# Kernel optimization log

Hardware: AMD Instinct MI355X
Metric: run time of the kernel (lower is better)

Reference implementation:

```python
import jax, jax.numpy as jnp
import numpy as np

E, D, H, K = 8, 1024, 4096, 2  # num_experts, input/output dim, hidden dim, top-k
B, S = 2, 2048


def setup_inputs() -> dict:
    key = jax.random.key(0)
    ks = jax.random.split(key, 5)
    s = 0.02
    return {
        "x": jax.random.normal(ks[0], (B, S, D), dtype=jnp.float32),
        "router_w": jax.random.normal(ks[1], (D, E), dtype=jnp.float32) * s,
        "router_b": jnp.zeros((E,), jnp.float32),
        "w1": jax.random.normal(ks[2], (E, D, H), dtype=jnp.float32) * s,
        "b1": jnp.zeros((E, H), jnp.float32),
        "w2": jax.random.normal(ks[3], (E, H, D), dtype=jnp.float32) * s,
        "b2": jnp.zeros((E, D), jnp.float32),
        "gamma": jnp.ones((E, D), jnp.float32),
        "beta": jnp.zeros((E, D), jnp.float32),
    }


def _layernorm(y, g, b, eps=1e-5):
    mu = y.mean(-1, keepdims=True)
    var = ((y - mu) ** 2).mean(-1, keepdims=True)
    return (y - mu) * jax.lax.rsqrt(var + eps) * g + b


def reference(x, router_w, router_b, w1, b1, w2, b2, gamma, beta):
    # Router
    router_logits = x @ router_w + router_b            # [B,S,E]
    probs = jax.nn.softmax(router_logits, axis=-1)
    topk_p, topk_i = jax.lax.top_k(probs, K)           # [B,S,K]
    topk_p = topk_p / topk_p.sum(-1, keepdims=True)

    # All experts over all tokens (equivalent to the masked dense loop,
    # since every expert op is per-token). Dropout = identity (eval).
    h = jax.nn.gelu(jnp.einsum('bsd,edh->ebsh', x, w1) + b1[:, None, None, :],
                    approximate=False)                  # [E,B,S,H]
    y = jnp.einsum('ebsh,ehd->ebsd', h, w2) + b2[:, None, None, :]
    eo = _layernorm(y + x[None], gamma[:, None, None, :], beta[:, None, None, :])  # [E,B,S,D]

    # Combine top-k experts per token
    eo = jnp.moveaxis(eo, 0, 2)                         # [B,S,E,D]
    gathered = jnp.take_along_axis(eo, topk_i[..., None], axis=2)  # [B,S,K,D]
    output = (gathered * topk_p[..., None]).sum(axis=2)            # [B,S,D]
    return output, router_logits
```

## Files before the change

### kernel.cpp

```cpp
#include <hip/hip_runtime.h>
#include <math.h>

#define NE 8
#define DD 1024
#define HH 4096
#define TT 4096
#define RR 8192

typedef __attribute__((ext_vector_type(8))) short short8;
typedef __attribute__((ext_vector_type(4))) float f32x4;

__device__ __forceinline__ unsigned short f2bf(float f) {
    unsigned int u = __float_as_uint(f);
    u += 0x7fffu + ((u >> 16) & 1u);
    return (unsigned short)(u >> 16);
}

__device__ __forceinline__ void async_copy16(void* lds, const void* g) {
    auto* lp = reinterpret_cast<__attribute__((address_space(3))) unsigned int*>(
        (unsigned int)(unsigned long long)(lds));
    auto* gp = reinterpret_cast<const __attribute__((address_space(1))) unsigned int*>(
        (unsigned long long)(g));
    __builtin_amdgcn_global_load_lds(gp, lp, 16, 0, 0);
}


__global__ void cvtx_kernel(const float* __restrict__ x, unsigned short* __restrict__ xb) {
    size_t i = (size_t)(blockIdx.x * 256 + threadIdx.x) * 4;
    float4 v = *(const float4*)&x[i];
    unsigned int lo = (unsigned int)f2bf(v.x) | ((unsigned int)f2bf(v.y) << 16);
    unsigned int hi = (unsigned int)f2bf(v.z) | ((unsigned int)f2bf(v.w) << 16);
    *(uint2*)&xb[i] = make_uint2(lo, hi);
}

__global__ __launch_bounds__(256) void transpose_swz_kernel(const float* __restrict__ src,
        unsigned short* __restrict__ dst, int K, int N) {
    const int e = blockIdx.z;
    src += (size_t)e * K * N;
    dst += (size_t)e * K * N;
    const int c0 = blockIdx.x * 64;
    const int r0 = blockIdx.y * 64;
    __shared__ unsigned short t[64][65];
    const int tid = threadIdx.x;
    const int rc4 = (tid & 15) * 4, rr = tid >> 4;
    #pragma unroll
    for (int i = 0; i < 4; i++) {
        int r = rr + i * 16;
        float4 v = *(const float4*)&src[(size_t)(r0 + r) * N + c0 + rc4];
        t[r][rc4]     = f2bf(v.x);
        t[r][rc4 + 1] = f2bf(v.y);
        t[r][rc4 + 2] = f2bf(v.z);
        t[r][rc4 + 3] = f2bf(v.w);
    }
    __syncthreads();
    const int n_local = tid & 63;
    const int n = c0 + n_local;
    const int nt = n >> 7, row = n & 127;
    const int Kdiv32 = K >> 5;
    #pragma unroll
    for (int it = 0; it < 2; it++) {
        int dg = (tid >> 6) + 4 * it;
        int kb = 2 * blockIdx.y + (dg >> 2);
        int q = dg & 3;
        unsigned short tmp[8];
        #pragma unroll
        for (int i = 0; i < 8; i++) tmp[i] = t[dg * 8 + i][n_local];
        size_t idx = ((((size_t)nt * Kdiv32 + kb) * 4 + q) * 128 + row) * 8;
        *(uint4*)&dst[idx] = *(uint4*)&tmp[0];
    }
}

__global__ void router_kernel(const float* __restrict__ x, const float* __restrict__ rw,
                              const float* __restrict__ rb, float* __restrict__ logits_out,
                              int* __restrict__ topk_e, float* __restrict__ topk_p,
                              int* __restrict__ counts) {
    const int t = blockIdx.x;
    const int tid = threadIdx.x;
    float4 xv = *(const float4*)&x[(size_t)t * DD + tid * 4];
    const float* rwp = rw + (size_t)(tid * 4) * NE;
    float acc[NE];
    #pragma unroll
    for (int e = 0; e < NE; e++) acc[e] = 0.f;
    float xs[4] = {xv.x, xv.y, xv.z, xv.w};
    #pragma unroll
    for (int i = 0; i < 4; i++) {
        #pragma unroll
        for (int e = 0; e < NE; e++) acc[e] += xs[i] * rwp[i * NE + e];
    }
    #pragma unroll
    for (int e = 0; e < NE; e++) {
        float v = acc[e];
        for (int off = 32; off > 0; off >>= 1) v += __shfl_down(v, off);
        acc[e] = v;
    }
    __shared__ float part[4][NE];
    if ((tid & 63) == 0) {
        #pragma unroll
        for (int e = 0; e < NE; e++) part[tid >> 6][e] = acc[e];
    }
    __syncthreads();
    if (tid == 0) {
        float lg[NE];
        #pragma unroll
        for (int e = 0; e < NE; e++)
            lg[e] = part[0][e] + part[1][e] + part[2][e] + part[3][e] + rb[e];
        #pragma unroll
        for (int e = 0; e < NE; e++) logits_out[(size_t)t * NE + e] = lg[e];
        float m = lg[0];
        #pragma unroll
        for (int e = 1; e < NE; e++) m = fmaxf(m, lg[e]);
        float pr[NE];
        #pragma unroll
        for (int e = 0; e < NE; e++) pr[e] = __expf(lg[e] - m);
        int i0 = 0;
        #pragma unroll
        for (int e = 1; e < NE; e++) if (pr[e] > pr[i0]) i0 = e;
        int i1 = (i0 == 0) ? 1 : 0;
        #pragma unroll
        for (int e = 0; e < NE; e++) if (e != i0 && pr[e] > pr[i1]) i1 = e;
        float p0 = pr[i0], p1 = pr[i1];
        float inv = 1.f / (p0 + p1);
        topk_e[t * 2] = i0;  topk_e[t * 2 + 1] = i1;
        topk_p[t * 2] = p0 * inv;  topk_p[t * 2 + 1] = p1 * inv;
        atomicAdd(&counts[i0], 1);
        atomicAdd(&counts[i1], 1);
    }
}

__global__ void prefix_kernel(const int* __restrict__ counts, int* __restrict__ offs,
                              int* __restrict__ cursor) {
    if (threadIdx.x == 0) {
        int a = 0;
        for (int e = 0; e < NE; e++) { offs[e] = a; cursor[e] = a; a += counts[e]; }
        offs[NE] = a;
    }
}

__global__ void scatter_kernel(const int* __restrict__ topk_e, int* __restrict__ cursor,
                               int* __restrict__ row_token, int* __restrict__ slot_of) {
    int i = blockIdx.x * 256 + threadIdx.x;
    int e = topk_e[i];
    int pos = atomicAdd(&cursor[e], 1);
    row_token[pos] = i >> 1;
    slot_of[i] = pos;
}

__global__ __launch_bounds__(256) void gemm1_kernel(
        const unsigned short* __restrict__ xb, const unsigned short* __restrict__ w1s,
        const float* __restrict__ b1, const int* __restrict__ offs,
        const int* __restrict__ row_token, unsigned short* __restrict__ hbuf) {
    const int e = blockIdx.z;
    const int r0 = offs[e];
    const int ne = offs[e + 1] - r0;
    const int rt = blockIdx.y;
    if (rt * 128 >= ne) return;
    const int nt = blockIdx.x;

    __shared__ __align__(16) unsigned short As[4096];
    __shared__ __align__(16) unsigned short Bs[4096];

    const int tid = threadIdx.x;
    const int lane = tid & 63;
    const int wv = tid >> 6;
    const int wr = (wv >> 1) * 64, wc = (wv & 1) * 64;
    const int m16 = lane & 15, q = lane >> 4;

    int ra = rt * 128 + lane;       ra = ra < ne ? ra : ne - 1;
    int rb = rt * 128 + 64 + lane;  rb = rb < ne ? rb : ne - 1;
    const unsigned short* ag0 = xb + (size_t)row_token[r0 + ra] * DD + wv * 8;
    const unsigned short* ag1 = xb + (size_t)row_token[r0 + rb] * DD + wv * 8;
    unsigned short* al0 = &As[wv * 1024 + lane * 8];
    unsigned short* al1 = &As[wv * 1024 + 512 + lane * 8];

    const unsigned short* bg = w1s + (size_t)e * HH * DD + (size_t)nt * (DD >> 5) * 4096
                               + wv * 1024 + lane * 8;
    unsigned short* bl0 = &Bs[wv * 1024 + lane * 8];
    unsigned short* bl1 = &Bs[wv * 1024 + 512 + lane * 8];

    f32x4 acc[4][4];
    f32x4 zero = {0.f, 0.f, 0.f, 0.f};
    #pragma unroll
    for (int i = 0; i < 4; i++)
        #pragma unroll
        for (int j = 0; j < 4; j++) acc[i][j] = zero;

    for (int k0 = 0; k0 < DD; k0 += 32) {
        async_copy16(al0, ag0);
        async_copy16(al1, ag1);
        async_copy16(bl0, bg);
        async_copy16(bl1, bg + 512);
        ag0 += 32; ag1 += 32; bg += 4096;
        __syncthreads();
        short8 af[4], bfr[4];
        #pragma unroll
        for (int i = 0; i < 4; i++) af[i] = *(const short8*)&As[q * 1024 + (wr + i * 16 + m16) * 8];
        #pragma unroll
        for (int j = 0; j < 4; j++) bfr[j] = *(const short8*)&Bs[q * 1024 + (wc + j * 16 + m16) * 8];
        #pragma unroll
        for (int i = 0; i < 4; i++)
            #pragma unroll
            for (int j = 0; j < 4; j++)
                acc[i][j] = __builtin_amdgcn_mfma_f32_16x16x32_bf16(af[i], bfr[j], acc[i][j], 0, 0, 0);
        __syncthreads();
    }

    const int n0 = nt * 128;
    float b1v[4];
    #pragma unroll
    for (int j = 0; j < 4; j++) b1v[j] = b1[(size_t)e * HH + n0 + wc + j * 16 + m16];
    #pragma unroll
    for (int i = 0; i < 4; i++) {
        #pragma unroll
        for (int rg = 0; rg < 4; rg++) {
            int rr = rt * 128 + wr + i * 16 + q * 4 + rg;
            if (rr < ne) {
                unsigned short* hrow = hbuf + (size_t)(r0 + rr) * HH;
                #pragma unroll
                for (int j = 0; j < 4; j++) {
                    int col = n0 + wc + j * 16 + m16;
                    float v = acc[i][j][rg] + b1v[j];
                    float g = 0.5f * v * (1.0f + erff(v * 0.70710678f));
                    hrow[col] = f2bf(g);
                }
            }
        }
    }
}

__global__ __launch_bounds__(256) void gemm2_kernel(
        const unsigned short* __restrict__ hbuf, const unsigned short* __restrict__ w2s,
        const float* __restrict__ b2, const float* __restrict__ x,
        const int* __restrict__ offs, const int* __restrict__ row_token,
        float* __restrict__ yp0, float* __restrict__ yp1) {
    const int e = blockIdx.z;
    const int r0 = offs[e];
    const int ne = offs[e + 1] - r0;
    const int rt = blockIdx.y;
    if (rt * 128 >= ne) return;
    const int chunk = blockIdx.x >> 3;
    const int nt = blockIdx.x & 7;
    const int kbase = chunk * (HH / 2);
    float* ybuf = chunk ? yp1 : yp0;

    __shared__ __align__(16) unsigned short As[4096];
    __shared__ __align__(16) unsigned short Bs[4096];

    const int tid = threadIdx.x;
    const int lane = tid & 63;
    const int wv = tid >> 6;
    const int wr = (wv >> 1) * 64, wc = (wv & 1) * 64;
    const int m16 = lane & 15, q = lane >> 4;

    int ra = rt * 128 + lane;       ra = ra < ne ? ra : ne - 1;
    int rb = rt * 128 + 64 + lane;  rb = rb < ne ? rb : ne - 1;
    const unsigned short* ag0 = hbuf + (size_t)(r0 + ra) * HH + kbase + wv * 8;
    const unsigned short* ag1 = hbuf + (size_t)(r0 + rb) * HH + kbase + wv * 8;
    unsigned short* al0 = &As[wv * 1024 + lane * 8];
    unsigned short* al1 = &As[wv * 1024 + 512 + lane * 8];

    const unsigned short* bg = w2s + (size_t)e * DD * HH + (size_t)nt * (HH >> 5) * 4096
                               + (size_t)(kbase >> 5) * 4096 + wv * 1024 + lane * 8;
    unsigned short* bl0 = &Bs[wv * 1024 + lane * 8];
    unsigned short* bl1 = &Bs[wv * 1024 + 512 + lane * 8];

    f32x4 acc[4][4];
    f32x4 zero = {0.f, 0.f, 0.f, 0.f};
    #pragma unroll
    for (int i = 0; i < 4; i++)
        #pragma unroll
        for (int j = 0; j < 4; j++) acc[i][j] = zero;

    for (int k0 = 0; k0 < HH / 2; k0 += 32) {
        async_copy16(al0, ag0);
        async_copy16(al1, ag1);
        async_copy16(bl0, bg);
        async_copy16(bl1, bg + 512);
        ag0 += 32; ag1 += 32; bg += 4096;
        __syncthreads();
        short8 af[4], bfr[4];
        #pragma unroll
        for (int i = 0; i < 4; i++) af[i] = *(const short8*)&As[q * 1024 + (wr + i * 16 + m16) * 8];
        #pragma unroll
        for (int j = 0; j < 4; j++) bfr[j] = *(const short8*)&Bs[q * 1024 + (wc + j * 16 + m16) * 8];
        #pragma unroll
        for (int i = 0; i < 4; i++)
            #pragma unroll
            for (int j = 0; j < 4; j++)
                acc[i][j] = __builtin_amdgcn_mfma_f32_16x16x32_bf16(af[i], bfr[j], acc[i][j], 0, 0, 0);
        __syncthreads();
    }

    const int n0 = nt * 128;
    float b2v[4] = {0.f, 0.f, 0.f, 0.f};
    if (chunk == 0) {
        #pragma unroll
        for (int j = 0; j < 4; j++) b2v[j] = b2[(size_t)e * DD + n0 + wc + j * 16 + m16];
    }
    #pragma unroll
    for (int i = 0; i < 4; i++) {
        #pragma unroll
        for (int rg = 0; rg < 4; rg++) {
            int rr = rt * 128 + wr + i * 16 + q * 4 + rg;
            if (rr < ne) {
                float* yrow = ybuf + (size_t)(r0 + rr) * DD;
                if (chunk == 0) {
                    int tok = row_token[r0 + rr];
                    const float* xrow = x + (size_t)tok * DD;
                    #pragma unroll
                    for (int j = 0; j < 4; j++) {
                        int col = n0 + wc + j * 16 + m16;
                        yrow[col] = acc[i][j][rg] + b2v[j] + xrow[col];
                    }
                } else {
                    #pragma unroll
                    for (int j = 0; j < 4; j++) {
                        int col = n0 + wc + j * 16 + m16;
                        yrow[col] = acc[i][j][rg];
                    }
                }
            }
        }
    }
}

__global__ void ln_combine_kernel(const float* __restrict__ yp0, const float* __restrict__ yp1,
                                  const int* __restrict__ slot_of,
                                  const int* __restrict__ topk_e, const float* __restrict__ topk_p,
                                  const float* __restrict__ gamma, const float* __restrict__ beta,
                                  float* __restrict__ out) {
    const int t = blockIdx.x;
    const int tid = threadIdx.x;
    __shared__ float ps[8];
    float4 o = {0.f, 0.f, 0.f, 0.f};
    #pragma unroll
    for (int k = 0; k < 2; k++) {
        int row = slot_of[t * 2 + k];
        int e = topk_e[t * 2 + k];
        float p = topk_p[t * 2 + k];
        float4 v0 = *(const float4*)&yp0[(size_t)row * DD + tid * 4];
        float4 v1 = *(const float4*)&yp1[(size_t)row * DD + tid * 4];
        float4 v = {v0.x + v1.x, v0.y + v1.y, v0.z + v1.z, v0.w + v1.w};
        float s = v.x + v.y + v.z + v.w;
        float sq = v.x * v.x + v.y * v.y + v.z * v.z + v.w * v.w;
        for (int off = 32; off > 0; off >>= 1) {
            s += __shfl_down(s, off);
            sq += __shfl_down(sq, off);
        }
        if ((tid & 63) == 0) { ps[tid >> 6] = s; ps[4 + (tid >> 6)] = sq; }
        __syncthreads();
        float fs = ps[0] + ps[1] + ps[2] + ps[3];
        float fq = ps[4] + ps[5] + ps[6] + ps[7];
        float mu = fs * (1.0f / DD);
        float var = fq * (1.0f / DD) - mu * mu;
        float rsig = rsqrtf(var + 1e-5f);
        float4 g = *(const float4*)&gamma[(size_t)e * DD + tid * 4];
        float4 bb = *(const float4*)&beta[(size_t)e * DD + tid * 4];
        o.x += p * ((v.x - mu) * rsig * g.x + bb.x);
        o.y += p * ((v.y - mu) * rsig * g.y + bb.y);
        o.z += p * ((v.z - mu) * rsig * g.z + bb.z);
        o.w += p * ((v.w - mu) * rsig * g.w + bb.w);
        __syncthreads();
    }
    *(float4*)&out[(size_t)t * DD + tid * 4] = o;
}

extern "C" void kernel_launch(void* const* d_in, const int* in_sizes, int n_in,
                              void* d_out, int out_size, void* d_ws, size_t ws_size,
                              hipStream_t stream) {
    const float* x     = (const float*)d_in[0];
    const float* rw    = (const float*)d_in[1];
    const float* rb    = (const float*)d_in[2];
    const float* w1    = (const float*)d_in[3];
    const float* b1    = (const float*)d_in[4];
    const float* w2    = (const float*)d_in[5];
    const float* b2    = (const float*)d_in[6];
    const float* gamma = (const float*)d_in[7];
    const float* beta  = (const float*)d_in[8];

    float* out    = (float*)d_out;
    float* logits = out + (size_t)TT * DD;

    char* w = (char*)d_ws;
    int*   counts    = (int*)(w + 0);
    int*   offs      = (int*)(w + 64);
    int*   cursor    = (int*)(w + 128);
    int*   topk_e    = (int*)(w + 4096);
    float* topk_p    = (float*)(w + 36864);
    int*   row_token = (int*)(w + 69632);
    int*   slot_of   = (int*)(w + 102400);
    unsigned short* xb   = (unsigned short*)(w + (size_t)1 * 1048576);
    unsigned short* w1s  = (unsigned short*)(w + (size_t)9 * 1048576);
    unsigned short* w2s  = (unsigned short*)(w + (size_t)73 * 1048576);
    unsigned short* hbuf = (unsigned short*)(w + (size_t)137 * 1048576);
    float*          yp0  = (float*)(w + (size_t)1 * 1048576);
    float*          yp1  = (float*)(w + (size_t)33 * 1048576);

    hipMemsetAsync(w, 0, 1024, stream);

    transpose_swz_kernel<<<dim3(HH / 64, DD / 64, NE), 256, 0, stream>>>(w1, w1s, DD, HH);
    transpose_swz_kernel<<<dim3(DD / 64, HH / 64, NE), 256, 0, stream>>>(w2, w2s, HH, DD);
    cvtx_kernel<<<4096, 256, 0, stream>>>(x, xb);
    router_kernel<<<TT, 256, 0, stream>>>(x, rw, rb, logits, topk_e, topk_p, counts);
    prefix_kernel<<<1, 64, 0, stream>>>(counts, offs, cursor);
    scatter_kernel<<<RR / 256, 256, 0, stream>>>(topk_e, cursor, row_token, slot_of);
    gemm1_kernel<<<dim3(HH / 128, 32, NE), 256, 0, stream>>>(xb, w1s, b1, offs, row_token, hbuf);
    gemm2_kernel<<<dim3(16, 32, NE), 256, 0, stream>>>(hbuf, w2s, b2, x, offs, row_token, yp0, yp1);
    ln_combine_kernel<<<TT, 256, 0, stream>>>(yp0, yp1, slot_of, topk_e, topk_p, gamma, beta, out);
}
```

Measured before the change: 814.1 us.

## Double-buffer LDS tiles in both expert GEMM k-loops

Both expert GEMMs now use two LDS buffers per operand. The next k-tile is loaded asynchronously into one buffer while MFMAs run on the other, using vmcnt waits and raw barriers instead of __syncthreads around every step. This hides global-load latency behind compute, at the cost of doubling LDS use (32KB per block), which may lower occupancy.

After: 758.6 us. -6.8%, faster.

```diff
diff --git a/kernel.cpp b/kernel.cpp
--- a/kernel.cpp
+++ b/kernel.cpp
@@ -145,6 +145,59 @@
     slot_of[i] = pos;
 }
 
+__device__ __forceinline__ void mfma_step(const unsigned short* Ab, const unsigned short* Bb,
+        int wr, int wc, int m16, int q, f32x4 (&acc)[4][4]) {
+    short8 af[4], bfr[4];
+    #pragma unroll
+    for (int i = 0; i < 4; i++) af[i] = *(const short8*)&Ab[q * 1024 + (wr + i * 16 + m16) * 8];
+    #pragma unroll
+    for (int j = 0; j < 4; j++) bfr[j] = *(const short8*)&Bb[q * 1024 + (wc + j * 16 + m16) * 8];
+    #pragma unroll
+    for (int i = 0; i < 4; i++)
+        #pragma unroll
+        for (int j = 0; j < 4; j++)
+            acc[i][j] = __builtin_amdgcn_mfma_f32_16x16x32_bf16(af[i], bfr[j], acc[i][j], 0, 0, 0);
+}
+
+template <int NK>
+__device__ __forceinline__ void kloop_db(
+        const unsigned short* ag0, const unsigned short* ag1, const unsigned short* bg,
+        unsigned short* As, unsigned short* Bs,
+        int wv, int lane, int wr, int wc, int m16, int q, f32x4 (&acc)[4][4]) {
+    unsigned short* alA = As + wv * 1024 + lane * 8;
+    unsigned short* blB = Bs + wv * 1024 + lane * 8;
+
+    async_copy16(alA, ag0);        async_copy16(alA + 512, ag1);
+    async_copy16(blB, bg);         async_copy16(blB + 512, bg + 512);
+    ag0 += 32; ag1 += 32; bg += 4096;
+
+    #pragma unroll 1
+    for (int it = 0; it < NK / 2 - 1; ++it) {
+        async_copy16(alA + 4096, ag0); async_copy16(alA + 4608, ag1);
+        async_copy16(blB + 4096, bg);  async_copy16(blB + 4608, bg + 512);
+        ag0 += 32; ag1 += 32; bg += 4096;
+        asm volatile("s_waitcnt vmcnt(4)" ::: "memory");
+        __builtin_amdgcn_s_barrier();
+        mfma_step(As, Bs, wr, wc, m16, q, acc);
+        __builtin_amdgcn_s_barrier();
+        async_copy16(alA, ag0);        async_copy16(alA + 512, ag1);
+        async_copy16(blB, bg);         async_copy16(blB + 512, bg + 512);
+        ag0 += 32; ag1 += 32; bg += 4096;
+        asm volatile("s_waitcnt vmcnt(4)" ::: "memory");
+        __builtin_amdgcn_s_barrier();
+        mfma_step(As + 4096, Bs + 4096, wr, wc, m16, q, acc);
+        __builtin_amdgcn_s_barrier();
+    }
+    async_copy16(alA + 4096, ag0); async_copy16(alA + 4608, ag1);
+    async_copy16(blB + 4096, bg);  async_copy16(blB + 4608, bg + 512);
+    asm volatile("s_waitcnt vmcnt(4)" ::: "memory");
+    __builtin_amdgcn_s_barrier();
+    mfma_step(As, Bs, wr, wc, m16, q, acc);
+    asm volatile("s_waitcnt vmcnt(0)" ::: "memory");
+    __builtin_amdgcn_s_barrier();
+    mfma_step(As + 4096, Bs + 4096, wr, wc, m16, q, acc);
+}
+
 __global__ __launch_bounds__(256) void gemm1_kernel(
         const unsigned short* __restrict__ xb, const unsigned short* __restrict__ w1s,
         const float* __restrict__ b1, const int* __restrict__ offs,
@@ -156,8 +209,8 @@
     if (rt * 128 >= ne) return;
     const int nt = blockIdx.x;
 
-    __shared__ __align__(16) unsigned short As[4096];
-    __shared__ __align__(16) unsigned short Bs[4096];
+    __shared__ __align__(16) unsigned short As[2][4096];
+    __shared__ __align__(16) unsigned short Bs[2][4096];
 
     const int tid = threadIdx.x;
     const int lane = tid & 63;
@@ -169,13 +222,9 @@
     int rb = rt * 128 + 64 + lane;  rb = rb < ne ? rb : ne - 1;
     const unsigned short* ag0 = xb + (size_t)row_token[r0 + ra] * DD + wv * 8;
     const unsigned short* ag1 = xb + (size_t)row_token[r0 + rb] * DD + wv * 8;
-    unsigned short* al0 = &As[wv * 1024 + lane * 8];
-    unsigned short* al1 = &As[wv * 1024 + 512 + lane * 8];
 
     const unsigned short* bg = w1s + (size_t)e * HH * DD + (size_t)nt * (DD >> 5) * 4096
                                + wv * 1024 + lane * 8;
-    unsigned short* bl0 = &Bs[wv * 1024 + lane * 8];
-    unsigned short* bl1 = &Bs[wv * 1024 + 512 + lane * 8];
 
     f32x4 acc[4][4];
     f32x4 zero = {0.f, 0.f, 0.f, 0.f};
@@ -184,25 +233,7 @@
         #pragma unroll
         for (int j = 0; j < 4; j++) acc[i][j] = zero;
 
-    for (int k0 = 0; k0 < DD; k0 += 32) {
-        async_copy16(al0, ag0);
-        async_copy16(al1, ag1);
-        async_copy16(bl0, bg);
-        async_copy16(bl1, bg + 512);
-        ag0 += 32; ag1 += 32; bg += 4096;
-        __syncthreads();
-        short8 af[4], bfr[4];
-        #pragma unroll
-        for (int i = 0; i < 4; i++) af[i] = *(const short8*)&As[q * 1024 + (wr + i * 16 + m16) * 8];
-        #pragma unroll
-        for (int j = 0; j < 4; j++) bfr[j] = *(const short8*)&Bs[q * 1024 + (wc + j * 16 + m16) * 8];
-        #pragma unroll
-        for (int i = 0; i < 4; i++)
-            #pragma unroll
-            for (int j = 0; j < 4; j++)
-                acc[i][j] = __builtin_amdgcn_mfma_f32_16x16x32_bf16(af[i], bfr[j], acc[i][j], 0, 0, 0);
-        __syncthreads();
-    }
+    kloop_db<DD / 32>(ag0, ag1, bg, &As[0][0], &Bs[0][0], wv, lane, wr, wc, m16, q, acc);
 
     const int n0 = nt * 128;
     float b1v[4];
@@ -242,8 +273,8 @@
     const int kbase = chunk * (HH / 2);
     float* ybuf = chunk ? yp1 : yp0;
 
-    __shared__ __align__(16) unsigned short As[4096];
-    __shared__ __align__(16) unsigned short Bs[4096];
+    __shared__ __align__(16) unsigned short As[2][4096];
+    __shared__ __align__(16) unsigned short Bs[2][4096];
 
     const int tid = threadIdx.x;
     const int lane = tid & 63;
@@ -255,13 +286,9 @@
     int rb = rt * 128 + 64 + lane;  rb = rb < ne ? rb : ne - 1;
     const unsigned short* ag0 = hbuf + (size_t)(r0 + ra) * HH + kbase + wv * 8;
     const unsigned short* ag1 = hbuf + (size_t)(r0 + rb) * HH + kbase + wv * 8;
-    unsigned short* al0 = &As[wv * 1024 + lane * 8];
-    unsigned short* al1 = &As[wv * 1024 + 512 + lane * 8];
 
     const unsigned short* bg = w2s + (size_t)e * DD * HH + (size_t)nt * (HH >> 5) * 4096
                                + (size_t)(kbase >> 5) * 4096 + wv * 1024 + lane * 8;
-    unsigned short* bl0 = &Bs[wv * 1024 + lane * 8];
-    unsigned short* bl1 = &Bs[wv * 1024 + 512 + lane * 8];
 
     f32x4 acc[4][4];
     f32x4 zero = {0.f, 0.f, 0.f, 0.f};
@@ -270,25 +297,7 @@
         #pragma unroll
         for (int j = 0; j < 4; j++) acc[i][j] = zero;
 
-    for (int k0 = 0; k0 < HH / 2; k0 += 32) {
-        async_copy16(al0, ag0);
-        async_copy16(al1, ag1);
-        async_copy16(bl0, bg);
-        async_copy16(bl1, bg + 512);
-        ag0 += 32; ag1 += 32; bg += 4096;
-        __syncthreads();
-        short8 af[4], bfr[4];
-        #pragma unroll
-        for (int i = 0; i < 4; i++) af[i] = *(const short8*)&As[q * 1024 + (wr + i * 16 + m16) * 8];
-        #pragma unroll
-        for (int j = 0; j < 4; j++) bfr[j] = *(const short8*)&Bs[q * 1024 + (wc + j * 16 + m16) * 8];
-        #pragma unroll
-        for (int i = 0; i < 4; i++)
-            #pragma unroll
-            for (int j = 0; j < 4; j++)
-                acc[i][j] = __builtin_amdgcn_mfma_f32_16x16x32_bf16(af[i], bfr[j], acc[i][j], 0, 0, 0);
-        __syncthreads();
-    }
+    kloop_db<(HH / 2) / 32>(ag0, ag1, bg, &As[0][0], &Bs[0][0], wv, lane, wr, wc, m16, q, acc);
 
     const int n0 = nt * 128;
     float b2v[4] = {0.f, 0.f, 0.f, 0.f};
```
